# Kernel tuning notes

Hardware: AMD Instinct MI355X
Metric: run time of the kernel (lower is better)

The kernel has to match this reference:

```python
import jax, jax.numpy as jnp
import numpy as np

B, S, D = 1, 4096, 768
H = 12
HD = D // H  # 64


def setup_inputs() -> dict:
    key = jax.random.key(0)
    ks = jax.random.split(key, 6)
    sc = 1.0 / np.sqrt(D)
    return {
        "x": jax.random.normal(ks[0], (B, S, D), dtype=jnp.float32),
        "wq": jax.random.normal(ks[1], (D, D), dtype=jnp.float32) * sc,
        "wk": jax.random.normal(ks[2], (D, D), dtype=jnp.float32) * sc,
        "wv": jax.random.normal(ks[3], (D, D), dtype=jnp.float32) * sc,
        "wo": jax.random.normal(ks[4], (D, D), dtype=jnp.float32) * sc,
        "bo": jax.random.normal(ks[5], (D,), dtype=jnp.float32) * 0.02,
    }


def reference(x, wq, wk, wv, wo, bo):
    b, n, _ = x.shape
    # projections (torch Linear: x @ W.T; here weights stored as (d_in, d_out))
    q = (x @ wq).reshape(b, n, H, HD).transpose(0, 2, 1, 3)  # b h n d
    k = (x @ wk).reshape(b, n, H, HD).transpose(0, 2, 1, 3)
    v = (x @ wv).reshape(b, n, H, HD).transpose(0, 2, 1, 3)
    scores = jnp.einsum("bhqd,bhkd->bhqk", q, k)
    causal = jnp.tril(jnp.ones((n, n), dtype=bool))  # True = keep
    scores = jnp.where(causal, scores, -jnp.inf)
    weights = jax.nn.softmax(scores / np.sqrt(HD), axis=-1)
    ctx = jnp.einsum("bhqk,bhkd->bhqd", weights, v)
    ctx = ctx.transpose(0, 2, 1, 3).reshape(b, n, D)
    return ctx @ wo + bo
```

## Files before the change

kernel.cpp:

```cpp
#include <hip/hip_runtime.h>


typedef short bf16x8 __attribute__((ext_vector_type(8)));
typedef float f32x4 __attribute__((ext_vector_type(4)));
typedef unsigned short u16;

static constexpr int S_LEN = 4096;
static constexpr int DIM   = 768;
static constexpr int NH    = 12;
static constexpr float QSCALE = 0.125f * 1.44269504088896340736f;

__device__ inline u16 f2bf(float f) {
  union { float f; unsigned int u; } v; v.f = f;
  unsigned int r = v.u + 0x7FFFu + ((v.u >> 16) & 1u);
  return (u16)(r >> 16);
}

__device__ inline void gload_lds16(const u16* g, u16* s) {
  __builtin_amdgcn_global_load_lds(
      (const __attribute__((address_space(1))) unsigned int*)g,
      (__attribute__((address_space(3))) unsigned int*)s, 16, 0, 0);
}

__global__ __launch_bounds__(256)
void prep_kernel(const float* __restrict__ x, const float* __restrict__ w0,
                 const float* __restrict__ w1, const float* __restrict__ w2,
                 const float* __restrict__ w3, u16* __restrict__ xb,
                 u16* __restrict__ t0, u16* __restrict__ t1,
                 u16* __restrict__ t2, u16* __restrict__ t3) {
  if (blockIdx.z == 4) {
    const size_t n = (size_t)S_LEN * DIM;
    const int id = blockIdx.y * 12 + blockIdx.x;
    const size_t stride = (size_t)144 * 256 * 8;
    for (size_t i = ((size_t)id * 256 + threadIdx.x) * 8; i < n; i += stride) {
      const float4 a = *(const float4*)(x + i);
      const float4 b = *(const float4*)(x + i + 4);
      bf16x8 o;
      o[0] = (short)f2bf(a.x); o[1] = (short)f2bf(a.y);
      o[2] = (short)f2bf(a.z); o[3] = (short)f2bf(a.w);
      o[4] = (short)f2bf(b.x); o[5] = (short)f2bf(b.y);
      o[6] = (short)f2bf(b.z); o[7] = (short)f2bf(b.w);
      *(bf16x8*)(xb + i) = o;
    }
    return;
  }
  __shared__ float T[64][65];
  const float* src; u16* dst;
  switch (blockIdx.z) {
    case 0: src = w0; dst = t0; break;
    case 1: src = w1; dst = t1; break;
    case 2: src = w2; dst = t2; break;
    default: src = w3; dst = t3; break;
  }
  const int k0 = blockIdx.y * 64, n0 = blockIdx.x * 64;
  const int r = threadIdx.x >> 2, c0 = (threadIdx.x & 3) * 16;
#pragma unroll
  for (int i = 0; i < 4; ++i) {
    const float4 v = *(const float4*)(src + (size_t)(k0 + r) * DIM + n0 + c0 + i * 4);
    T[r][c0 + i * 4 + 0] = v.x;
    T[r][c0 + i * 4 + 1] = v.y;
    T[r][c0 + i * 4 + 2] = v.z;
    T[r][c0 + i * 4 + 3] = v.w;
  }
  __syncthreads();
  bf16x8 o0, o1;
#pragma unroll
  for (int i = 0; i < 8; ++i) {
    o0[i] = (short)f2bf(T[c0 + i][r]);
    o1[i] = (short)f2bf(T[c0 + 8 + i][r]);
  }
  *(bf16x8*)(dst + (size_t)(n0 + r) * DIM + k0 + c0) = o0;
  *(bf16x8*)(dst + (size_t)(n0 + r) * DIM + k0 + c0 + 8) = o1;
}

template <int MODE>
__global__ __launch_bounds__(256)
void mfma_gemm_kernel(const u16* __restrict__ A, const u16* __restrict__ Bq,
                      const u16* __restrict__ Bk, const u16* __restrict__ Bv,
                      const float* __restrict__ bias, u16* __restrict__ Qb,
                      u16* __restrict__ Kb, u16* __restrict__ VT,
                      float* __restrict__ Out) {
  constexpr int MT = (MODE == 0) ? 4 : 2;
  constexpr int BM = MT * 32;
  __shared__ __align__(16) u16 Al[BM * 64];
  __shared__ __align__(16) u16 Bl[96 * 64];

  const int tid  = threadIdx.x;
  const int wv   = tid >> 6;
  const int lane = tid & 63;
  const int quad = lane >> 4;
  const int l16  = lane & 15;
  const int wr = wv >> 1, wc = wv & 1;
  const int m0 = blockIdx.y * BM;
  const int n0 = blockIdx.x * 96;

  int wi = 0, nb = n0;
  const u16* BT = Bq;
  if (MODE == 0) {
    wi = n0 / DIM;
    nb = n0 - wi * DIM;
    BT = (wi == 0) ? Bq : (wi == 1) ? Bk : Bv;
  }

  const int sr8 = lane >> 3;
  const int sc  = ((lane & 7) ^ sr8) * 8;
  const int key = l16 & 7;

  const bool swp = (MODE == 1) || (wi < 2);

  f32x4 acc[MT][3] = {};

  for (int k0 = 0; k0 < DIM; k0 += 64) {
    __syncthreads();
#pragma unroll
    for (int j = 0; j < MT; ++j)
      gload_lds16(A + (size_t)(m0 + wv * (BM / 4) + j * 8 + sr8) * DIM + k0 + sc,
                  &Al[(wv * (BM / 4) + j * 8) * 64]);
#pragma unroll
    for (int j = 0; j < 3; ++j)
      gload_lds16(BT + (size_t)(nb + wv * 24 + j * 8 + sr8) * DIM + k0 + sc,
                  &Bl[(wv * 24 + j * 8) * 64]);
    __syncthreads();

#pragma unroll
    for (int kh = 0; kh < 2; ++kh) {
      const int cb = kh * 4;
      bf16x8 af[MT], bfr[3];
#pragma unroll
      for (int mt = 0; mt < MT; ++mt) {
        const int row = wr * (BM / 2) + mt * 16 + l16;
        af[mt] = *(const bf16x8*)&Al[row * 64 + ((cb + quad) ^ key) * 8];
      }
#pragma unroll
      for (int nt = 0; nt < 3; ++nt) {
        const int row = wc * 48 + nt * 16 + l16;
        bfr[nt] = *(const bf16x8*)&Bl[row * 64 + ((cb + quad) ^ key) * 8];
      }
      if (swp) {
#pragma unroll
        for (int mt = 0; mt < MT; ++mt)
#pragma unroll
          for (int nt = 0; nt < 3; ++nt)
            acc[mt][nt] = __builtin_amdgcn_mfma_f32_16x16x32_bf16(
                bfr[nt], af[mt], acc[mt][nt], 0, 0, 0);
      } else {
#pragma unroll
        for (int mt = 0; mt < MT; ++mt)
#pragma unroll
          for (int nt = 0; nt < 3; ++nt)
            acc[mt][nt] = __builtin_amdgcn_mfma_f32_16x16x32_bf16(
                af[mt], bfr[nt], acc[mt][nt], 0, 0, 0);
      }
    }
  }

  if (MODE == 0 && wi >= 2) {
#pragma unroll
    for (int mt = 0; mt < MT; ++mt) {
#pragma unroll
      for (int nt = 0; nt < 3; ++nt) {
        const int row  = m0 + wr * (BM / 2) + mt * 16 + quad * 4;
        const int ncol = nb + wc * 48 + nt * 16 + l16;
        u16 pk[4];
#pragma unroll
        for (int r = 0; r < 4; ++r) pk[r] = f2bf(acc[mt][nt][r]);
        unsigned long long v;
        __builtin_memcpy(&v, pk, 8);
        *(unsigned long long*)(VT + (size_t)ncol * S_LEN + row) = v;
      }
    }
  } else if (MODE == 0) {
    u16* dst = (wi == 0) ? Qb : Kb;
    const float sc_out = (wi == 0) ? QSCALE : 1.0f;
#pragma unroll
    for (int mt = 0; mt < MT; ++mt) {
#pragma unroll
      for (int nt = 0; nt < 3; ++nt) {
        const int row = m0 + wr * (BM / 2) + mt * 16 + l16;
        const int ncb = nb + wc * 48 + nt * 16 + quad * 4;
        u16 pk[4];
#pragma unroll
        for (int r = 0; r < 4; ++r) pk[r] = f2bf(acc[mt][nt][r] * sc_out);
        unsigned long long v;
        __builtin_memcpy(&v, pk, 8);
        *(unsigned long long*)(dst + (size_t)row * DIM + ncb) = v;
      }
    }
  } else {
#pragma unroll
    for (int mt = 0; mt < MT; ++mt) {
#pragma unroll
      for (int nt = 0; nt < 3; ++nt) {
        const int row = m0 + wr * (BM / 2) + mt * 16 + l16;
        const int ncb = n0 + wc * 48 + nt * 16 + quad * 4;
        const float4 b4 = *(const float4*)(bias + ncb);
        float4 ov;
        ov.x = acc[mt][nt][0] + b4.x;
        ov.y = acc[mt][nt][1] + b4.y;
        ov.z = acc[mt][nt][2] + b4.z;
        ov.w = acc[mt][nt][3] + b4.w;
        *(float4*)(Out + (size_t)row * DIM + ncb) = ov;
      }
    }
  }
}

__global__ __launch_bounds__(256)
void attn_mfma_kernel(const u16* __restrict__ Qb, const u16* __restrict__ Kb,
                      const u16* __restrict__ VTb, u16* __restrict__ ctx) {
  __shared__ __align__(16) u16 KVl[128 * 64 + 64 * 128];
  __shared__ __align__(16) u16 Pl[4][16 * 72];
  __shared__ float4 lbuf[4][64];

  u16* Kl = KVl;
  u16* Vl = KVl + 128 * 64;

  const int tid  = threadIdx.x;
  const int w    = tid >> 6;
  const int lane = tid & 63;
  const int quad = lane >> 4;
  const int l16  = lane & 15;
  const int qw   = w >> 1;
  const int kw   = w & 1;
  const int key  = l16 & 7;

  const int id = blockIdx.x;
  const int rc = id & 7, slot = id >> 3;
  const int h  = (slot < 64) ? rc : 8 + (rc >> 1);
  const int bx = (slot < 64) ? slot : ((rc & 1) * 32 + (slot - 64));

  const int sr8  = lane >> 3;
  const int scK  = ((lane & 7) ^ sr8) * 8;
  const int sr16 = lane >> 4;

#pragma unroll 1
  for (int side = 0; side < 2; ++side) {
    const int qt = side ? (127 - bx) : bx;
    const int q0 = qt * 32;

    const u16* qptr = Qb + (size_t)(q0 + qw * 16 + l16) * DIM + h * 64 + quad * 8;
    const bf16x8 aq0 = *(const bf16x8*)(qptr);
    const bf16x8 aq1 = *(const bf16x8*)(qptr + 32);

    f32x4 o[4] = {};
    float l_r[4] = {};

    const int nkt = qt / 2 + 1;
    const int niter = (nkt + 1) >> 1;
    const int my_last = nkt - 1;

#pragma unroll 1
    for (int i = 0; i < niter; ++i) {
      const int k0g = i * 128;
      __syncthreads();
#pragma unroll
      for (int j = 0; j < 4; ++j)
        gload_lds16(Kb + (size_t)(k0g + w * 32 + j * 8 + sr8) * DIM + h * 64 + scK,
                    &Kl[(w * 32 + j * 8) * 64]);
#pragma unroll
      for (int j = 0; j < 4; ++j) {
        const int vrow = w * 16 + j * 4 + sr16;
        const int vcol = ((lane & 15) ^ (vrow & 7)) * 8;
        gload_lds16(VTb + (size_t)(h * 64 + vrow) * S_LEN + k0g + vcol,
                    &Vl[(w * 16 + j * 4) * 128]);
      }
      __syncthreads();

      const int kt_w = 2 * i + kw;
      if (kt_w < nkt) {
        f32x4 s[4];
#pragma unroll
        for (int t = 0; t < 4; ++t) {
          const int row = kw * 64 + t * 16 + l16;
          const bf16x8 bk0 = *(const bf16x8*)&Kl[row * 64 + (quad ^ key) * 8];
          const bf16x8 bk1 = *(const bf16x8*)&Kl[row * 64 + ((quad ^ 4) ^ key) * 8];
          s[t] = __builtin_amdgcn_mfma_f32_16x16x32_bf16(
              aq0, bk0, f32x4{0.f, 0.f, 0.f, 0.f}, 0, 0, 0);
          s[t] = __builtin_amdgcn_mfma_f32_16x16x32_bf16(aq1, bk1, s[t], 0, 0, 0);
        }

        if (kt_w == my_last) {
#pragma unroll
          for (int t = 0; t < 4; ++t)
#pragma unroll
            for (int r = 0; r < 4; ++r) {
              const int kvg = k0g + kw * 64 + t * 16 + l16;
              const int qg  = q0 + qw * 16 + quad * 4 + r;
              float p = __builtin_amdgcn_exp2f(s[t][r]);
              if (kvg > qg) p = 0.f;
              l_r[r] += p;
              Pl[w][(quad * 4 + r) * 72 + t * 16 + l16] =
                  (u16)((__float_as_uint(p) + 0x8000u) >> 16);
            }
        } else {
#pragma unroll
          for (int t = 0; t < 4; ++t)
#pragma unroll
            for (int r = 0; r < 4; ++r) {
              const float p = __builtin_amdgcn_exp2f(s[t][r]);
              l_r[r] += p;
              Pl[w][(quad * 4 + r) * 72 + t * 16 + l16] =
                  (u16)((__float_as_uint(p) + 0x8000u) >> 16);
            }
        }

        const bf16x8 pa0 = *(const bf16x8*)&Pl[w][l16 * 72 + quad * 8];
        const bf16x8 pa1 = *(const bf16x8*)&Pl[w][l16 * 72 + 32 + quad * 8];
#pragma unroll
        for (int t = 0; t < 4; ++t) {
          const int row = t * 16 + l16;
          const int c0 = (kw * 8 + quad) ^ key;
          const int c1 = (kw * 8 + quad + 4) ^ key;
          const bf16x8 vb0 = *(const bf16x8*)&Vl[row * 128 + c0 * 8];
          const bf16x8 vb1 = *(const bf16x8*)&Vl[row * 128 + c1 * 8];
          o[t] = __builtin_amdgcn_mfma_f32_16x16x32_bf16(pa0, vb0, o[t], 0, 0, 0);
          o[t] = __builtin_amdgcn_mfma_f32_16x16x32_bf16(pa1, vb1, o[t], 0, 0, 0);
        }
      }
    }

    __syncthreads();
    float* Obuf = (float*)KVl;
#pragma unroll
    for (int t = 0; t < 4; ++t)
      *(f32x4*)&Obuf[(w * 64 + lane) * 20 + t * 4] = o[t];
    lbuf[w][lane] = float4{l_r[0], l_r[1], l_r[2], l_r[3]};
    __syncthreads();
#pragma unroll
    for (int t = 0; t < 4; ++t) {
      const f32x4 po = *(const f32x4*)&Obuf[((w ^ 1) * 64 + lane) * 20 + t * 4];
      o[t] += po;
    }
    {
      const float4 pl = lbuf[w ^ 1][lane];
      l_r[0] += pl.x; l_r[1] += pl.y; l_r[2] += pl.z; l_r[3] += pl.w;
    }

    if (kw == 0) {
#pragma unroll
      for (int r = 0; r < 4; ++r) {
        float l = l_r[r];
        l += __shfl_xor(l, 1);
        l += __shfl_xor(l, 2);
        l += __shfl_xor(l, 4);
        l += __shfl_xor(l, 8);
        const float inv = 1.f / l;
        const int row = q0 + qw * 16 + quad * 4 + r;
#pragma unroll
        for (int t = 0; t < 4; ++t)
          ctx[(size_t)row * DIM + h * 64 + t * 16 + l16] = f2bf(o[t][r] * inv);
      }
    }
  }
}

extern "C" void kernel_launch(void* const* d_in, const int* in_sizes, int n_in,
                              void* d_out, int out_size, void* d_ws,
                              size_t ws_size, hipStream_t stream) {
  const float* x  = (const float*)d_in[0];
  const float* wq = (const float*)d_in[1];
  const float* wk = (const float*)d_in[2];
  const float* wv = (const float*)d_in[3];
  const float* wo = (const float*)d_in[4];
  const float* bo = (const float*)d_in[5];

  const size_t n_x = (size_t)S_LEN * DIM;
  const size_t n_w = (size_t)DIM * DIM;
  u16* xb  = (u16*)d_ws;
  u16* wtq = xb + n_x;
  u16* wtk = wtq + n_w;
  u16* wtv = wtk + n_w;
  u16* wto = wtv + n_w;
  u16* Qb  = wto + n_w;
  u16* Kb  = Qb + n_x;
  u16* VTb = Kb + n_x;
  u16* ctx = VTb + n_x;

  prep_kernel<<<dim3(12, 12, 5), 256, 0, stream>>>(
      x, wq, wk, wv, wo, xb, wtq, wtk, wtv, wto);

  mfma_gemm_kernel<0><<<dim3(24, 32), 256, 0, stream>>>(
      xb, wtq, wtk, wtv, nullptr, Qb, Kb, VTb, nullptr);

  attn_mfma_kernel<<<dim3(768), 256, 0, stream>>>(Qb, Kb, VTb, ctx);

  mfma_gemm_kernel<1><<<dim3(8, 64), 256, 0, stream>>>(
      ctx, wto, nullptr, nullptr, bo, nullptr, nullptr, nullptr, (float*)d_out);
}
```

Baseline: 174.5 us.

## Prefetch next K/V tile into LDS while computing from register-staged tile

Result: no change. 177.2 us (+1.6%).

```diff
diff --git a/kernel.cpp b/kernel.cpp
--- a/kernel.cpp
+++ b/kernel.cpp
@@ -205,7 +205,7 @@
   }
 }
 
-__global__ __launch_bounds__(256)
+__global__ __launch_bounds__(256, 3)
 void attn_mfma_kernel(const u16* __restrict__ Qb, const u16* __restrict__ Kb,
                       const u16* __restrict__ VTb, u16* __restrict__ ctx) {
   __shared__ __align__(16) u16 KVl[128 * 64 + 64 * 128];
@@ -249,34 +249,65 @@
     const int niter = (nkt + 1) >> 1;
     const int my_last = nkt - 1;
 
+    __syncthreads();
+#pragma unroll
+    for (int j = 0; j < 4; ++j)
+      gload_lds16(Kb + (size_t)(w * 32 + j * 8 + sr8) * DIM + h * 64 + scK,
+                  &Kl[(w * 32 + j * 8) * 64]);
+#pragma unroll
+    for (int j = 0; j < 4; ++j) {
+      const int vrow = w * 16 + j * 4 + sr16;
+      const int vcol = ((lane & 15) ^ (vrow & 7)) * 8;
+      gload_lds16(VTb + (size_t)(h * 64 + vrow) * S_LEN + vcol,
+                  &Vl[(w * 16 + j * 4) * 128]);
+    }
+
 #pragma unroll 1
     for (int i = 0; i < niter; ++i) {
       const int k0g = i * 128;
       __syncthreads();
-#pragma unroll
-      for (int j = 0; j < 4; ++j)
-        gload_lds16(Kb + (size_t)(k0g + w * 32 + j * 8 + sr8) * DIM + h * 64 + scK,
-                    &Kl[(w * 32 + j * 8) * 64]);
-#pragma unroll
-      for (int j = 0; j < 4; ++j) {
-        const int vrow = w * 16 + j * 4 + sr16;
-        const int vcol = ((lane & 15) ^ (vrow & 7)) * 8;
-        gload_lds16(VTb + (size_t)(h * 64 + vrow) * S_LEN + k0g + vcol,
-                    &Vl[(w * 16 + j * 4) * 128]);
+
+      const int kt_w = 2 * i + kw;
+      const bool active = (kt_w < nkt);
+
+      bf16x8 bk0[4], bk1[4], vb0[4], vb1[4];
+      if (active) {
+#pragma unroll
+        for (int t = 0; t < 4; ++t) {
+          const int krow = kw * 64 + t * 16 + l16;
+          bk0[t] = *(const bf16x8*)&Kl[krow * 64 + (quad ^ key) * 8];
+          bk1[t] = *(const bf16x8*)&Kl[krow * 64 + ((quad ^ 4) ^ key) * 8];
+          const int vrow = t * 16 + l16;
+          const int c0 = (kw * 8 + quad) ^ key;
+          const int c1 = (kw * 8 + quad + 4) ^ key;
+          vb0[t] = *(const bf16x8*)&Vl[vrow * 128 + c0 * 8];
+          vb1[t] = *(const bf16x8*)&Vl[vrow * 128 + c1 * 8];
+        }
       }
       __syncthreads();
 
-      const int kt_w = 2 * i + kw;
-      if (kt_w < nkt) {
+      if (i + 1 < niter) {
+        const int kn = k0g + 128;
+#pragma unroll
+        for (int j = 0; j < 4; ++j)
+          gload_lds16(Kb + (size_t)(kn + w * 32 + j * 8 + sr8) * DIM + h * 64 + scK,
+                      &Kl[(w * 32 + j * 8) * 64]);
+#pragma unroll
+        for (int j = 0; j < 4; ++j) {
+          const int vrow = w * 16 + j * 4 + sr16;
+          const int vcol = ((lane & 15) ^ (vrow & 7)) * 8;
+          gload_lds16(VTb + (size_t)(h * 64 + vrow) * S_LEN + kn + vcol,
+                      &Vl[(w * 16 + j * 4) * 128]);
+        }
+      }
+
+      if (active) {
         f32x4 s[4];
 #pragma unroll
         for (int t = 0; t < 4; ++t) {
-          const int row = kw * 64 + t * 16 + l16;
-          const bf16x8 bk0 = *(const bf16x8*)&Kl[row * 64 + (quad ^ key) * 8];
-          const bf16x8 bk1 = *(const bf16x8*)&Kl[row * 64 + ((quad ^ 4) ^ key) * 8];
           s[t] = __builtin_amdgcn_mfma_f32_16x16x32_bf16(
-              aq0, bk0, f32x4{0.f, 0.f, 0.f, 0.f}, 0, 0, 0);
-          s[t] = __builtin_amdgcn_mfma_f32_16x16x32_bf16(aq1, bk1, s[t], 0, 0, 0);
+              aq0, bk0[t], f32x4{0.f, 0.f, 0.f, 0.f}, 0, 0, 0);
+          s[t] = __builtin_amdgcn_mfma_f32_16x16x32_bf16(aq1, bk1[t], s[t], 0, 0, 0);
         }
 
         if (kt_w == my_last) {
@@ -308,18 +339,12 @@
         const bf16x8 pa1 = *(const bf16x8*)&Pl[w][l16 * 72 + 32 + quad * 8];
 #pragma unroll
         for (int t = 0; t < 4; ++t) {
-          const int row = t * 16 + l16;
-          const int c0 = (kw * 8 + quad) ^ key;
-          const int c1 = (kw * 8 + quad + 4) ^ key;
-          const bf16x8 vb0 = *(const bf16x8*)&Vl[row * 128 + c0 * 8];
-          const bf16x8 vb1 = *(const bf16x8*)&Vl[row * 128 + c1 * 8];
-          o[t] = __builtin_amdgcn_mfma_f32_16x16x32_bf16(pa0, vb0, o[t], 0, 0, 0);
-          o[t] = __builtin_amdgcn_mfma_f32_16x16x32_bf16(pa1, vb1, o[t], 0, 0, 0);
+          o[t] = __builtin_amdgcn_mfma_f32_16x16x32_bf16(pa0, vb0[t], o[t], 0, 0, 0);
+          o[t] = __builtin_amdgcn_mfma_f32_16x16x32_bf16(pa1, vb1[t], o[t], 0, 0, 0);
         }
       }
     }
 
-    __syncthreads();
     float* Obuf = (float*)KVl;
 #pragma unroll
     for (int t = 0; t < 4; ++t)
```
